# Kernel optimization log

Hardware: AMD Instinct MI355X
Metric: run time of the kernel (lower is better)

## Reference

```python
import jax, jax.numpy as jnp
import numpy as np

N = 50000
E = 800000
IN = 256
HEADS = 8
C = 32  # out_size // heads
OUT = HEADS * C
NEG_SLOPE = 0.2
LN_EPS = 1e-5


def setup_inputs() -> dict:
    key = jax.random.key(0)
    ks = jax.random.split(key, 6)
    x = jax.random.normal(ks[0], (N, IN), dtype=jnp.float32)
    edge_index = jax.random.randint(ks[1], (2, E), 0, N, dtype=jnp.int64)
    W = jax.random.normal(ks[2], (IN, OUT), dtype=jnp.float32) / np.sqrt(IN)
    att_src = jax.random.normal(ks[3], (HEADS, C), dtype=jnp.float32) / np.sqrt(C)
    att_dst = jax.random.normal(ks[4], (HEADS, C), dtype=jnp.float32) / np.sqrt(C)
    bias = jnp.zeros((OUT,), dtype=jnp.float32)
    ln_gamma = jnp.ones((OUT,), dtype=jnp.float32)
    ln_beta = jnp.zeros((OUT,), dtype=jnp.float32)
    return {"x": x, "edge_index": edge_index, "W": W, "att_src": att_src,
            "att_dst": att_dst, "bias": bias, "ln_gamma": ln_gamma, "ln_beta": ln_beta}


def _gat_layer(x, src, dst, W, att_src, att_dst, bias, ln_gamma, ln_beta):
    n = x.shape[0]
    h = (x @ W).reshape(n, HEADS, C)                      # [N,H,C]
    a_src = jnp.sum(h * att_src[None], axis=-1)           # [N,H]
    a_dst = jnp.sum(h * att_dst[None], axis=-1)           # [N,H]
    e = a_src[src] + a_dst[dst]                           # [Etot,H]
    e = jnp.where(e > 0, e, NEG_SLOPE * e)                # LeakyReLU(0.2)
    # segment softmax over incoming edges of each dst node
    emax = jax.lax.stop_gradient(jax.ops.segment_max(e, dst, num_segments=n))
    ex = jnp.exp(e - emax[dst])
    denom = jax.ops.segment_sum(ex, dst, num_segments=n)
    alpha = ex / denom[dst]                               # [Etot,H]
    msg = h[src] * alpha[:, :, None]                      # [Etot,H,C]
    out = jax.ops.segment_sum(msg, dst, num_segments=n).reshape(n, OUT) + bias
    # LayerNorm
    mu = jnp.mean(out, axis=-1, keepdims=True)
    var = jnp.var(out, axis=-1, keepdims=True)
    out = (out - mu) * jax.lax.rsqrt(var + LN_EPS) * ln_gamma + ln_beta
    return jax.nn.relu(out)


def reference(x, edge_index, W, att_src, att_dst, bias, ln_gamma, ln_beta):
    n = x.shape[0]
    loops = jnp.arange(n, dtype=edge_index.dtype)
    src = jnp.concatenate([edge_index[0], loops])  # PyG GATConv adds self-loops
    dst = jnp.concatenate([edge_index[1], loops])
    return _gat_layer(x, src, dst, W, att_src, att_dst, bias, ln_gamma, ln_beta)
```

## Files before the change

kernel.cpp:

```cpp
#include <hip/hip_runtime.h>

#define NEG 0.2f
#define ELLW 64

typedef __attribute__((ext_vector_type(8))) __bf16 bf16x8;
typedef __attribute__((ext_vector_type(4))) float f32x4;

__device__ __forceinline__ unsigned short f2bf(float f) {
    unsigned int u = __float_as_uint(f);
    u += 0x7FFFu + ((u >> 16) & 1u);
    return (unsigned short)(u >> 16);
}

__global__ __launch_bounds__(256) void prep_kernel(const float* __restrict__ W,
                                                   unsigned short* __restrict__ Wt,
                                                   int* __restrict__ len, int N) {
    int n = blockIdx.x, k = threadIdx.x;
    Wt[n * 256 + k] = f2bf(W[k * 256 + n]);
    int idx = n * 256 + k;
    if (idx < N) len[idx] = 0;
}

struct SmemGemm { unsigned short A[64][40]; unsigned short B[256][40]; };
struct SmemEpi  { float asrc[64][9]; float adst[64][9]; };
union SmemU { SmemGemm g; SmemEpi e; };

__global__ __launch_bounds__(256) void gemm_ell(const float* __restrict__ x,
                                                const unsigned short* __restrict__ Wt,
                                                unsigned short* __restrict__ h,
                                                const float* __restrict__ att_src,
                                                const float* __restrict__ att_dst,
                                                float* __restrict__ a_src,
                                                float* __restrict__ a_dst, int nrows, int G,
                                                const int* __restrict__ ei,
                                                int* __restrict__ len,
                                                int* __restrict__ ell, int E) {
    __shared__ SmemU sm;

    if (blockIdx.x >= G) {
        int e = (blockIdx.x - G) * 256 + threadIdx.x;
        if (e < E) {
            int s = ei[e], d = ei[E + e];
            int slot = atomicAdd(&len[d], 1);
            if (slot < ELLW) ell[d * ELLW + slot] = s;
        }
        return;
    }

    int t = threadIdx.x;
    int lane = t & 63, wave = t >> 6;
    int row0 = blockIdx.x * 64;

    f32x4 acc[4][4] = {};

    for (int kk = 0; kk < 8; ++kk) {
        int k0 = kk * 32;
        {
            int r = t >> 2, cg = (t & 3) * 8;
            int gr = row0 + r;
            float4 v0 = make_float4(0.f, 0.f, 0.f, 0.f), v1 = v0;
            if (gr < nrows) {
                const float* p = x + (size_t)gr * 256 + k0 + cg;
                v0 = *(const float4*)p;
                v1 = *(const float4*)(p + 4);
            }
            unsigned long long p0 = (unsigned long long)f2bf(v0.x)
                                  | ((unsigned long long)f2bf(v0.y) << 16)
                                  | ((unsigned long long)f2bf(v0.z) << 32)
                                  | ((unsigned long long)f2bf(v0.w) << 48);
            unsigned long long p1 = (unsigned long long)f2bf(v1.x)
                                  | ((unsigned long long)f2bf(v1.y) << 16)
                                  | ((unsigned long long)f2bf(v1.z) << 32)
                                  | ((unsigned long long)f2bf(v1.w) << 48);
            *(unsigned long long*)&sm.g.A[r][cg]     = p0;
            *(unsigned long long*)&sm.g.A[r][cg + 4] = p1;
        }
        {
            const uint4* src = (const uint4*)(Wt + (size_t)t * 256 + k0);
            uint4 b0 = src[0], b1 = src[1], b2 = src[2], b3 = src[3];
            *(uint4*)&sm.g.B[t][0]  = b0;
            *(uint4*)&sm.g.B[t][8]  = b1;
            *(uint4*)&sm.g.B[t][16] = b2;
            *(uint4*)&sm.g.B[t][24] = b3;
        }
        __syncthreads();

        int fr = lane & 15, fk = (lane >> 4) * 8;
        bf16x8 a[4];
#pragma unroll
        for (int mi = 0; mi < 4; ++mi) a[mi] = *(const bf16x8*)&sm.g.A[mi * 16 + fr][fk];
#pragma unroll
        for (int ni = 0; ni < 4; ++ni) {
            bf16x8 b = *(const bf16x8*)&sm.g.B[wave * 64 + ni * 16 + fr][fk];
#pragma unroll
            for (int mi = 0; mi < 4; ++mi)
                acc[mi][ni] = __builtin_amdgcn_mfma_f32_16x16x32_bf16(a[mi], b, acc[mi][ni], 0, 0, 0);
        }
        __syncthreads();
    }

    int cr = (lane >> 4) * 4;
    int cc = lane & 15;
#pragma unroll
    for (int mi = 0; mi < 4; ++mi)
#pragma unroll
        for (int ni = 0; ni < 4; ++ni)
#pragma unroll
            for (int r = 0; r < 4; ++r) {
                int row = row0 + mi * 16 + cr + r;
                int col = wave * 64 + ni * 16 + cc;
                if (row < nrows) h[(size_t)row * 256 + col] = f2bf(acc[mi][ni][r]);
            }

    float avs[4], avd[4];
#pragma unroll
    for (int ni = 0; ni < 4; ++ni) {
        int col = wave * 64 + ni * 16 + cc;
        avs[ni] = att_src[col];
        avd[ni] = att_dst[col];
    }
#pragma unroll
    for (int mi = 0; mi < 4; ++mi)
#pragma unroll
        for (int r = 0; r < 4; ++r) {
            float s0 = acc[mi][0][r] * avs[0] + acc[mi][1][r] * avs[1];
            float s1 = acc[mi][2][r] * avs[2] + acc[mi][3][r] * avs[3];
            float d0 = acc[mi][0][r] * avd[0] + acc[mi][1][r] * avd[1];
            float d1 = acc[mi][2][r] * avd[2] + acc[mi][3][r] * avd[3];
#pragma unroll
            for (int o = 1; o < 16; o <<= 1) {
                s0 += __shfl_xor(s0, o, 64);
                s1 += __shfl_xor(s1, o, 64);
                d0 += __shfl_xor(d0, o, 64);
                d1 += __shfl_xor(d1, o, 64);
            }
            if (cc == 0) {
                int row = mi * 16 + cr + r;
                sm.e.asrc[row][wave * 2 + 0] = s0;
                sm.e.asrc[row][wave * 2 + 1] = s1;
                sm.e.adst[row][wave * 2 + 0] = d0;
                sm.e.adst[row][wave * 2 + 1] = d1;
            }
        }
    __syncthreads();
    for (int idx = t; idx < 512; idx += 256) {
        int row = idx >> 3, hd = idx & 7;
        if (row0 + row < nrows) {
            a_src[(size_t)(row0 + row) * 8 + hd] = sm.e.asrc[row][hd];
            a_dst[(size_t)(row0 + row) * 8 + hd] = sm.e.adst[row][hd];
        }
    }
}

__global__ __launch_bounds__(256) void agg_kernel(const unsigned short* __restrict__ h,
                                                  const float* __restrict__ a_src,
                                                  const float* __restrict__ a_dst,
                                                  const int* __restrict__ len,
                                                  const int* __restrict__ ell,
                                                  const float* __restrict__ bias,
                                                  const float* __restrict__ gamma,
                                                  const float* __restrict__ beta,
                                                  float* __restrict__ out) {
    int i = blockIdx.x;
    int t = threadIdx.x;
    int lane = t & 63, wave = t >> 6;
    int hh = t & 7, jj = t >> 3;
    int deg = len[i];
    deg = deg < ELLW ? deg : ELLW;

    __shared__ float al_buf[ELLW][8];
    __shared__ int   s_buf[ELLW];
    __shared__ float wred[4][8];
    __shared__ float ginv[8];
    __shared__ float al_self[8];
    __shared__ float partial[8][256];
    __shared__ float lnred[4][2];

    float adh = a_dst[i * 8 + hh];
    float es = a_src[i * 8 + hh] + adh;
    es = es > 0.f ? es : NEG * es;
    float esx = __expf(es);
    float sm = (jj == 0) ? esx : 0.f;
    if (t < 8) al_self[t] = esx;

#pragma unroll
    for (int it = 0; it < 2; ++it) {
        int j = it * 32 + jj;
        if (j < deg) {
            int s = ell[i * ELLW + j];
            if (hh == 0) s_buf[j] = s;
            float e = a_src[s * 8 + hh] + adh;
            e = e > 0.f ? e : NEG * e;
            float v = __expf(e);
            al_buf[j][hh] = v;
            sm += v;
        }
    }
    sm += __shfl_xor(sm, 8, 64);
    sm += __shfl_xor(sm, 16, 64);
    sm += __shfl_xor(sm, 32, 64);
    if (lane < 8) wred[wave][lane] = sm;
    __syncthreads();
    if (t < 8) ginv[t] = 1.0f / (wred[0][t] + wred[1][t] + wred[2][t] + wred[3][t]);
    __syncthreads();

    int sub = lane >> 5, l5 = lane & 31;
    int p = wave * 2 + sub;
    int c0 = l5 * 8;
    int hl = l5 >> 2;
    float invd = ginv[hl];
    f32x4 a0 = {0.f, 0.f, 0.f, 0.f}, a1 = {0.f, 0.f, 0.f, 0.f};
    for (int j = p; j < deg; j += 8) {
        int s = s_buf[j];
        float alpha = al_buf[j][hl] * invd;
        uint4 u = *(const uint4*)(h + (size_t)s * 256 + c0);
        a0[0] = fmaf(alpha, __uint_as_float(u.x << 16), a0[0]);
        a0[1] = fmaf(alpha, __uint_as_float(u.x & 0xffff0000u), a0[1]);
        a0[2] = fmaf(alpha, __uint_as_float(u.y << 16), a0[2]);
        a0[3] = fmaf(alpha, __uint_as_float(u.y & 0xffff0000u), a0[3]);
        a1[0] = fmaf(alpha, __uint_as_float(u.z << 16), a1[0]);
        a1[1] = fmaf(alpha, __uint_as_float(u.z & 0xffff0000u), a1[1]);
        a1[2] = fmaf(alpha, __uint_as_float(u.w << 16), a1[2]);
        a1[3] = fmaf(alpha, __uint_as_float(u.w & 0xffff0000u), a1[3]);
    }
    if (p == 7) {
        float alpha = al_self[hl] * invd;
        uint4 u = *(const uint4*)(h + (size_t)i * 256 + c0);
        a0[0] = fmaf(alpha, __uint_as_float(u.x << 16), a0[0]);
        a0[1] = fmaf(alpha, __uint_as_float(u.x & 0xffff0000u), a0[1]);
        a0[2] = fmaf(alpha, __uint_as_float(u.y << 16), a0[2]);
        a0[3] = fmaf(alpha, __uint_as_float(u.y & 0xffff0000u), a0[3]);
        a1[0] = fmaf(alpha, __uint_as_float(u.z << 16), a1[0]);
        a1[1] = fmaf(alpha, __uint_as_float(u.z & 0xffff0000u), a1[1]);
        a1[2] = fmaf(alpha, __uint_as_float(u.w << 16), a1[2]);
        a1[3] = fmaf(alpha, __uint_as_float(u.w & 0xffff0000u), a1[3]);
    }
    *(f32x4*)&partial[p][c0]     = a0;
    *(f32x4*)&partial[p][c0 + 4] = a1;
    __syncthreads();

    float o = bias[t];
#pragma unroll
    for (int q = 0; q < 8; ++q) o += partial[q][t];

    float s1 = o, s2 = o * o;
#pragma unroll
    for (int off = 32; off >= 1; off >>= 1) {
        s1 += __shfl_xor(s1, off, 64);
        s2 += __shfl_xor(s2, off, 64);
    }
    if (lane == 0) { lnred[wave][0] = s1; lnred[wave][1] = s2; }
    __syncthreads();
    float S1 = lnred[0][0] + lnred[1][0] + lnred[2][0] + lnred[3][0];
    float S2 = lnred[0][1] + lnred[1][1] + lnred[2][1] + lnred[3][1];
    float mean = S1 * (1.f / 256.f);
    float var = S2 * (1.f / 256.f) - mean * mean;
    float rstd = rsqrtf(var + 1e-5f);
    float val = (o - mean) * rstd * gamma[t] + beta[t];
    val = fmaxf(val, 0.f);
    out[(size_t)i * 256 + t] = val;
}

extern "C" void kernel_launch(void* const* d_in, const int* in_sizes, int n_in,
                              void* d_out, int out_size, void* d_ws, size_t ws_size,
                              hipStream_t stream) {
    const float* x       = (const float*)d_in[0];
    const int*   ei      = (const int*)d_in[1];
    const float* W       = (const float*)d_in[2];
    const float* att_src = (const float*)d_in[3];
    const float* att_dst = (const float*)d_in[4];
    const float* bias    = (const float*)d_in[5];
    const float* gamma   = (const float*)d_in[6];
    const float* beta    = (const float*)d_in[7];

    int N = in_sizes[0] / 256;
    int E = in_sizes[1] / 2;
    int G = (N + 63) / 64;
    int EB = (E + 255) / 256;

    char* ws = (char*)d_ws;
    size_t off = 0;
    auto alloc = [&](size_t bytes) -> void* {
        void* p = ws + off;
        off += (bytes + 255) & ~(size_t)255;
        return p;
    };
    unsigned short* Wt     = (unsigned short*)alloc((size_t)256 * 256 * 2);
    unsigned short* h      = (unsigned short*)alloc((size_t)N * 256 * 2);
    float*          a_src_ = (float*)alloc((size_t)N * 8 * 4);
    float*          a_dst_ = (float*)alloc((size_t)N * 8 * 4);
    int*            len    = (int*)alloc((size_t)N * 4);
    int*            ell    = (int*)alloc((size_t)N * ELLW * 4);

    prep_kernel<<<256, 256, 0, stream>>>(W, Wt, len, N);
    gemm_ell<<<G + EB, 256, 0, stream>>>(x, Wt, h, att_src, att_dst, a_src_, a_dst_, N, G,
                                         ei, len, ell, E);
    agg_kernel<<<N, 256, 0, stream>>>(h, a_src_, a_dst_, len, ell, bias, gamma, beta,
                                      (float*)d_out);
}
```

Before: 280.3 us.

## Map one wave per node in aggregation, replacing block syncs with shuffles

The aggregation kernel now gives each destination node a single 64-lane wave, with four nodes per block, instead of a whole 256-thread block. The per-node reductions (softmax denominator, partial-sum combine, LayerNorm stats) become wave shuffles rather than shared-memory buffers with __syncthreads. Neighbor indices stay in registers and are broadcast by shuffle. The neighbor-row gather is software-prefetched one step ahead, and bias, gamma and beta are loaded as float4. Fewer lanes per node means less in-flight gather parallelism for each node in exchange for less synchronization and higher occupancy.

```diff
diff --git a/kernel.cpp b/kernel.cpp
--- a/kernel.cpp
+++ b/kernel.cpp
@@ -152,113 +152,141 @@
     }
 }
 
-__global__ __launch_bounds__(256) void agg_kernel(const unsigned short* __restrict__ h,
-                                                  const float* __restrict__ a_src,
-                                                  const float* __restrict__ a_dst,
-                                                  const int* __restrict__ len,
-                                                  const int* __restrict__ ell,
-                                                  const float* __restrict__ bias,
-                                                  const float* __restrict__ gamma,
-                                                  const float* __restrict__ beta,
-                                                  float* __restrict__ out) {
-    int i = blockIdx.x;
-    int t = threadIdx.x;
-    int lane = t & 63, wave = t >> 6;
-    int hh = t & 7, jj = t >> 3;
+__device__ __forceinline__ void fma8(f32x4& a0, f32x4& a1, float al, uint4 u) {
+    a0[0] = fmaf(al, __uint_as_float(u.x << 16),         a0[0]);
+    a0[1] = fmaf(al, __uint_as_float(u.x & 0xffff0000u), a0[1]);
+    a0[2] = fmaf(al, __uint_as_float(u.y << 16),         a0[2]);
+    a0[3] = fmaf(al, __uint_as_float(u.y & 0xffff0000u), a0[3]);
+    a1[0] = fmaf(al, __uint_as_float(u.z << 16),         a1[0]);
+    a1[1] = fmaf(al, __uint_as_float(u.z & 0xffff0000u), a1[1]);
+    a1[2] = fmaf(al, __uint_as_float(u.w << 16),         a1[2]);
+    a1[3] = fmaf(al, __uint_as_float(u.w & 0xffff0000u), a1[3]);
+}
+
+__global__ __launch_bounds__(256, 6) void agg_kernel(const unsigned short* __restrict__ h,
+                                                     const float* __restrict__ a_src,
+                                                     const float* __restrict__ a_dst,
+                                                     const int* __restrict__ len,
+                                                     const int* __restrict__ ell,
+                                                     const float* __restrict__ bias,
+                                                     const float* __restrict__ gamma,
+                                                     const float* __restrict__ beta,
+                                                     float* __restrict__ out, int N) {
+    __shared__ float alL[4][ELLW][8];
+
+    int lane = threadIdx.x & 63, wave = threadIdx.x >> 6;
+    int i = blockIdx.x * 4 + wave;
+    if (i >= N) return;
+
+    volatile float (*al)[8] = alL[wave];
+
     int deg = len[i];
     deg = deg < ELLW ? deg : ELLW;
 
-    __shared__ float al_buf[ELLW][8];
-    __shared__ int   s_buf[ELLW];
-    __shared__ float wred[4][8];
-    __shared__ float ginv[8];
-    __shared__ float al_self[8];
-    __shared__ float partial[8][256];
-    __shared__ float lnred[4][2];
-
+    int sreg = (lane < deg) ? ell[i * ELLW + lane] : 0;
+
+    int hh = lane & 7, jj = lane >> 3;
     float adh = a_dst[i * 8 + hh];
     float es = a_src[i * 8 + hh] + adh;
     es = es > 0.f ? es : NEG * es;
-    float esx = __expf(es);
-    float sm = (jj == 0) ? esx : 0.f;
-    if (t < 8) al_self[t] = esx;
-
-#pragma unroll
-    for (int it = 0; it < 2; ++it) {
-        int j = it * 32 + jj;
+    float selfexp = __expf(es);
+
+    float sum = (jj == 0) ? selfexp : 0.f;
+    for (int jb = 0; jb < deg; jb += 8) {
+        int j = jb + jj;
+        int jc = j < deg ? j : deg - 1;
+        int s = __shfl(sreg, jc, 64);
+        float e = a_src[s * 8 + hh] + adh;
+        e = e > 0.f ? e : NEG * e;
+        float v = __expf(e);
         if (j < deg) {
-            int s = ell[i * ELLW + j];
-            if (hh == 0) s_buf[j] = s;
-            float e = a_src[s * 8 + hh] + adh;
-            e = e > 0.f ? e : NEG * e;
-            float v = __expf(e);
-            al_buf[j][hh] = v;
-            sm += v;
-        }
-    }
-    sm += __shfl_xor(sm, 8, 64);
-    sm += __shfl_xor(sm, 16, 64);
-    sm += __shfl_xor(sm, 32, 64);
-    if (lane < 8) wred[wave][lane] = sm;
-    __syncthreads();
-    if (t < 8) ginv[t] = 1.0f / (wred[0][t] + wred[1][t] + wred[2][t] + wred[3][t]);
-    __syncthreads();
+            al[j][hh] = v;
+            sum += v;
+        }
+    }
+    sum += __shfl_xor(sum, 8, 64);
+    sum += __shfl_xor(sum, 16, 64);
+    sum += __shfl_xor(sum, 32, 64);
+    float ginv = 1.0f / sum;
+
+    __builtin_amdgcn_wave_barrier();
 
     int sub = lane >> 5, l5 = lane & 31;
-    int p = wave * 2 + sub;
     int c0 = l5 * 8;
     int hl = l5 >> 2;
-    float invd = ginv[hl];
+    float gv = __shfl(ginv, hl, 64);
+    float sv = __shfl(selfexp, hl, 64);
+
     f32x4 a0 = {0.f, 0.f, 0.f, 0.f}, a1 = {0.f, 0.f, 0.f, 0.f};
-    for (int j = p; j < deg; j += 8) {
-        int s = s_buf[j];
-        float alpha = al_buf[j][hl] * invd;
-        uint4 u = *(const uint4*)(h + (size_t)s * 256 + c0);
-        a0[0] = fmaf(alpha, __uint_as_float(u.x << 16), a0[0]);
-        a0[1] = fmaf(alpha, __uint_as_float(u.x & 0xffff0000u), a0[1]);
-        a0[2] = fmaf(alpha, __uint_as_float(u.y << 16), a0[2]);
-        a0[3] = fmaf(alpha, __uint_as_float(u.y & 0xffff0000u), a0[3]);
-        a1[0] = fmaf(alpha, __uint_as_float(u.z << 16), a1[0]);
-        a1[1] = fmaf(alpha, __uint_as_float(u.z & 0xffff0000u), a1[1]);
-        a1[2] = fmaf(alpha, __uint_as_float(u.w << 16), a1[2]);
-        a1[3] = fmaf(alpha, __uint_as_float(u.w & 0xffff0000u), a1[3]);
-    }
-    if (p == 7) {
-        float alpha = al_self[hl] * invd;
-        uint4 u = *(const uint4*)(h + (size_t)i * 256 + c0);
-        a0[0] = fmaf(alpha, __uint_as_float(u.x << 16), a0[0]);
-        a0[1] = fmaf(alpha, __uint_as_float(u.x & 0xffff0000u), a0[1]);
-        a0[2] = fmaf(alpha, __uint_as_float(u.y << 16), a0[2]);
-        a0[3] = fmaf(alpha, __uint_as_float(u.y & 0xffff0000u), a0[3]);
-        a1[0] = fmaf(alpha, __uint_as_float(u.z << 16), a1[0]);
-        a1[1] = fmaf(alpha, __uint_as_float(u.z & 0xffff0000u), a1[1]);
-        a1[2] = fmaf(alpha, __uint_as_float(u.w << 16), a1[2]);
-        a1[3] = fmaf(alpha, __uint_as_float(u.w & 0xffff0000u), a1[3]);
-    }
-    *(f32x4*)&partial[p][c0]     = a0;
-    *(f32x4*)&partial[p][c0 + 4] = a1;
-    __syncthreads();
-
-    float o = bias[t];
-#pragma unroll
-    for (int q = 0; q < 8; ++q) o += partial[q][t];
-
-    float s1 = o, s2 = o * o;
-#pragma unroll
-    for (int off = 32; off >= 1; off >>= 1) {
+    int dm1 = deg - 1;
+    float alpha = 0.f;
+    uint4 u = make_uint4(0u, 0u, 0u, 0u);
+    if (deg > 0) {
+        int j = sub;
+        int jc = j < deg ? j : dm1;
+        int s = __shfl(sreg, jc, 64);
+        alpha = (j < deg ? al[jc][hl] : 0.f) * gv;
+        u = *(const uint4*)(h + (size_t)s * 256 + c0);
+    }
+    for (int jb = 0; jb < deg; jb += 2) {
+        float alpha_c = alpha;
+        uint4 u_c = u;
+        int jbn = jb + 2;
+        if (jbn < deg) {
+            int j = jbn + sub;
+            int jc = j < deg ? j : dm1;
+            int s = __shfl(sreg, jc, 64);
+            alpha = (j < deg ? al[jc][hl] : 0.f) * gv;
+            u = *(const uint4*)(h + (size_t)s * 256 + c0);
+        }
+        fma8(a0, a1, alpha_c, u_c);
+    }
+    {
+        float alphaS = (sub == 1) ? sv * gv : 0.f;
+        uint4 us = *(const uint4*)(h + (size_t)i * 256 + c0);
+        fma8(a0, a1, alphaS, us);
+    }
+#pragma unroll
+    for (int k = 0; k < 4; ++k) {
+        a0[k] += __shfl_xor(a0[k], 32, 64);
+        a1[k] += __shfl_xor(a1[k], 32, 64);
+    }
+
+    float4 b0 = *(const float4*)(bias + c0);
+    float4 b1 = *(const float4*)(bias + c0 + 4);
+    float o0 = a0[0] + b0.x, o1 = a0[1] + b0.y, o2 = a0[2] + b0.z, o3 = a0[3] + b0.w;
+    float o4 = a1[0] + b1.x, o5 = a1[1] + b1.y, o6 = a1[2] + b1.z, o7 = a1[3] + b1.w;
+
+    float s1 = o0 + o1 + o2 + o3 + o4 + o5 + o6 + o7;
+    float s2 = o0 * o0 + o1 * o1 + o2 * o2 + o3 * o3
+             + o4 * o4 + o5 * o5 + o6 * o6 + o7 * o7;
+#pragma unroll
+    for (int off = 16; off >= 1; off >>= 1) {
         s1 += __shfl_xor(s1, off, 64);
         s2 += __shfl_xor(s2, off, 64);
     }
-    if (lane == 0) { lnred[wave][0] = s1; lnred[wave][1] = s2; }
-    __syncthreads();
-    float S1 = lnred[0][0] + lnred[1][0] + lnred[2][0] + lnred[3][0];
-    float S2 = lnred[0][1] + lnred[1][1] + lnred[2][1] + lnred[3][1];
-    float mean = S1 * (1.f / 256.f);
-    float var = S2 * (1.f / 256.f) - mean * mean;
+    float mean = s1 * (1.f / 256.f);
+    float var = s2 * (1.f / 256.f) - mean * mean;
     float rstd = rsqrtf(var + 1e-5f);
-    float val = (o - mean) * rstd * gamma[t] + beta[t];
-    val = fmaxf(val, 0.f);
-    out[(size_t)i * 256 + t] = val;
+
+    float4 g0 = *(const float4*)(gamma + c0);
+    float4 g1 = *(const float4*)(gamma + c0 + 4);
+    float4 t0 = *(const float4*)(beta + c0);
+    float4 t1 = *(const float4*)(beta + c0 + 4);
+
+    f32x4 w0, w1;
+    w0[0] = fmaxf((o0 - mean) * rstd * g0.x + t0.x, 0.f);
+    w0[1] = fmaxf((o1 - mean) * rstd * g0.y + t0.y, 0.f);
+    w0[2] = fmaxf((o2 - mean) * rstd * g0.z + t0.z, 0.f);
+    w0[3] = fmaxf((o3 - mean) * rstd * g0.w + t0.w, 0.f);
+    w1[0] = fmaxf((o4 - mean) * rstd * g1.x + t1.x, 0.f);
+    w1[1] = fmaxf((o5 - mean) * rstd * g1.y + t1.y, 0.f);
+    w1[2] = fmaxf((o6 - mean) * rstd * g1.z + t1.z, 0.f);
+    w1[3] = fmaxf((o7 - mean) * rstd * g1.w + t1.w, 0.f);
+
+    float* op = out + (size_t)i * 256 + c0;
+    if (sub == 0) *(f32x4*)op       = w0;
+    else          *(f32x4*)(op + 4) = w1;
 }
 
 extern "C" void kernel_launch(void* const* d_in, const int* in_sizes, int n_in,
@@ -295,6 +323,6 @@
     prep_kernel<<<256, 256, 0, stream>>>(W, Wt, len, N);
     gemm_ell<<<G + EB, 256, 0, stream>>>(x, Wt, h, att_src, att_dst, a_src_, a_dst_, N, G,
                                          ei, len, ell, E);
-    agg_kernel<<<N, 256, 0, stream>>>(h, a_src_, a_dst_, len, ell, bias, gamma, beta,
-                                      (float*)d_out);
-}
+    agg_kernel<<<(N + 3) / 4, 256, 0, stream>>>(h, a_src_, a_dst_, len, ell, bias, gamma, beta,
+                                                (float*)d_out, N);
+}
```

After: 243.4 us. -13.2%, faster.
